# Performance work log

Hardware: AMD Instinct MI355X
Metric: run time of the kernel (lower is better)

## Reference

```python
import jax, jax.numpy as jnp
import numpy as np

B, S, D = 8, 1024, 768
H, HD = 12, 64
FF = 3072
EPS = 1e-5


def layernorm(x, w, b):
    mu = jnp.mean(x, axis=-1, keepdims=True)
    var = jnp.mean(jnp.square(x - mu), axis=-1, keepdims=True)
    return (x - mu) / jnp.sqrt(var + EPS) * w + b


def setup_inputs() -> dict:
    key = jax.random.key(0)
    ks = jax.random.split(key, 16)
    s_in = 1.0 / np.sqrt(D)
    s_p = 1.0 / np.sqrt(H * HD)
    s_ff = 1.0 / np.sqrt(FF)
    return {
        "x": jax.random.normal(ks[0], (B, S, D), dtype=jnp.float32),
        "ln1_w": jnp.ones((D,), jnp.float32),
        "ln1_b": jnp.zeros((D,), jnp.float32),
        "Wq": jax.random.uniform(ks[1], (H, D, HD), jnp.float32, -s_in, s_in),
        "bq": jax.random.uniform(ks[2], (H, HD), jnp.float32, -s_in, s_in),
        "Wk": jax.random.uniform(ks[3], (H, D, HD), jnp.float32, -s_in, s_in),
        "bk": jax.random.uniform(ks[4], (H, HD), jnp.float32, -s_in, s_in),
        "Wv": jax.random.uniform(ks[5], (H, D, HD), jnp.float32, -s_in, s_in),
        "bv": jax.random.uniform(ks[6], (H, HD), jnp.float32, -s_in, s_in),
        "Wp": jax.random.uniform(ks[7], (H * HD, D), jnp.float32, -s_p, s_p),
        "bp": jax.random.uniform(ks[8], (D,), jnp.float32, -s_p, s_p),
        "ln2_w": jnp.ones((D,), jnp.float32),
        "ln2_b": jnp.zeros((D,), jnp.float32),
        "W1": jax.random.uniform(ks[9], (D, FF), jnp.float32, -s_in, s_in),
        "b1": jax.random.uniform(ks[10], (FF,), jnp.float32, -s_in, s_in),
        "W2": jax.random.uniform(ks[11], (FF, D), jnp.float32, -s_ff, s_ff),
        "b2": jax.random.uniform(ks[12], (D,), jnp.float32, -s_ff, s_ff),
    }


def reference(x, ln1_w, ln1_b, Wq, bq, Wk, bk, Wv, bv, Wp, bp,
              ln2_w, ln2_b, W1, b1, W2, b2):
    gelu = lambda t: jax.nn.gelu(t, approximate=False)
    # --- multi-head self attention (NOTE: original never applies scale) ---
    y = layernorm(x, ln1_w, ln1_b)                       # [B,S,D]
    q = jnp.einsum('bsd,hde->bhse', y, Wq) + bq[:, None, :][None]
    k = jnp.einsum('bsd,hde->bhse', y, Wk) + bk[:, None, :][None]
    v = jnp.einsum('bsd,hde->bhse', y, Wv) + bv[:, None, :][None]
    attn = jax.nn.softmax(jnp.einsum('bhse,bhte->bhst', q, k), axis=-1)
    out = jnp.einsum('bhst,bhte->bhse', attn, v)         # [B,H,S,HD]
    out = out.transpose(0, 2, 1, 3).reshape(x.shape[0], x.shape[1], -1)  # concat heads
    y = gelu(out @ Wp + bp)                              # projection + GELU
    x = x + y                                            # residual 1
    # --- MLP block ---
    h = layernorm(x, ln2_w, ln2_b)
    h = gelu(h @ W1 + b1)
    h = gelu(h @ W2 + b2)
    return x + h                                         # residual 2
```

## Files before the change

kernel.cpp:

```cpp
#include <hip/hip_runtime.h>
#include <hip/hip_bf16.h>
#include <math.h>

#define BB 8
#define SS 1024
#define DD 768
#define HH 12
#define HDD 64
#define FFF 3072
#define NROW (BB*SS)
#define QKVN (3*DD)

typedef __hip_bfloat16 bf16;
typedef __bf16 bf16x8 __attribute__((ext_vector_type(8)));
typedef float floatx4 __attribute__((ext_vector_type(4)));

__device__ __forceinline__ float gelu_fast(float x) {
    float u = x * fmaf(0.07135481627f, x * x, 1.595769122f);
    float e = __expf(u);
    return x * e * __builtin_amdgcn_rcpf(e + 1.0f);
}

__device__ __forceinline__ unsigned short f2bfbits(float f) {
    bf16 h = __float2bfloat16(f);
    return __builtin_bit_cast(unsigned short, h);
}

__device__ __forceinline__ void gload16(const void* g, void* l) {
    __builtin_amdgcn_global_load_lds(
        (const __attribute__((address_space(1))) unsigned int*)g,
        (__attribute__((address_space(3))) unsigned int*)l, 16, 0, 0);
}

__global__ __launch_bounds__(256) void ln_kernel(const float* __restrict__ x,
                                                 const float* __restrict__ w,
                                                 const float* __restrict__ b,
                                                 bf16* __restrict__ y) {
    int row = blockIdx.x;
    const float* xr = x + (size_t)row * DD;
    bf16* yr = y + (size_t)row * DD;
    int tid = threadIdx.x;
    float v0 = xr[tid], v1 = xr[tid + 256], v2 = xr[tid + 512];
    __shared__ float red[256], red2[256];
    red[tid]  = v0 + v1 + v2;
    red2[tid] = v0*v0 + v1*v1 + v2*v2;
    __syncthreads();
    for (int off = 128; off > 0; off >>= 1) {
        if (tid < off) { red[tid] += red[tid+off]; red2[tid] += red2[tid+off]; }
        __syncthreads();
    }
    float mu  = red[0] * (1.0f / DD);
    float var = red2[0] * (1.0f / DD) - mu * mu;
    float inv = rsqrtf(var + 1e-5f);
    yr[tid]       = __float2bfloat16((v0 - mu) * inv * w[tid]       + b[tid]);
    yr[tid + 256] = __float2bfloat16((v1 - mu) * inv * w[tid + 256] + b[tid + 256]);
    yr[tid + 512] = __float2bfloat16((v2 - mu) * inv * w[tid + 512] + b[tid + 512]);
}

__global__ __launch_bounds__(256) void prep_kernel(
    const float* __restrict__ Wq, const float* __restrict__ Wk,
    const float* __restrict__ Wv, const float* __restrict__ Wp,
    const float* __restrict__ W1, const float* __restrict__ W2,
    const float* __restrict__ bq, const float* __restrict__ bk,
    const float* __restrict__ bv,
    bf16* __restrict__ Wqkvt, bf16* __restrict__ Wpt,
    bf16* __restrict__ W1t, bf16* __restrict__ W2t, float* __restrict__ bqkv)
{
    int id = blockIdx.x;
    if (id >= 6912) {
        int i = (id - 6912) * 256 + threadIdx.x;
        if (i < DD) { bqkv[i] = bq[i]; bqkv[DD + i] = bk[i]; bqkv[2*DD + i] = bv[i]; }
        return;
    }
    const float* src; bf16* dst; int K, N, hmode, local;
    if (id < 1728)      { K = DD;  N = DD;  hmode = 1; local = id % 576;
                          src = (id < 576) ? Wq : (id < 1152 ? Wk : Wv);
                          dst = Wqkvt + (size_t)(id / 576) * DD * DD; }
    else if (id < 2304) { K = DD;  N = DD;  hmode = 0; local = id - 1728; src = Wp; dst = Wpt; }
    else if (id < 4608) { K = DD;  N = FFF; hmode = 0; local = id - 2304; src = W1; dst = W1t; }
    else                { K = FFF; N = DD;  hmode = 0; local = id - 4608; src = W2; dst = W2t; }
    int ktiles = K / 32;
    int k0 = (local % ktiles) * 32, n0 = (local / ktiles) * 32;
    __shared__ float t[32][33];
    int tx = threadIdx.x & 31, ty4 = threadIdx.x >> 5;
    #pragma unroll
    for (int i = 0; i < 4; i++) {
        int k = k0 + ty4 * 4 + i;
        int n = n0 + tx;
        size_t si = hmode ? ((size_t)(n >> 6) * K * 64 + (size_t)k * 64 + (n & 63))
                          : ((size_t)k * N + n);
        t[ty4 * 4 + i][tx] = src[si];
    }
    __syncthreads();
    #pragma unroll
    for (int i = 0; i < 4; i++) {
        int n = n0 + ty4 * 4 + i;
        int k = k0 + tx;
        dst[(size_t)n * K + k] = __float2bfloat16(t[tx][ty4 * 4 + i]);
    }
}

template<int MT, int KH>
__global__ __launch_bounds__(256) void mfma_gemm(
    const bf16* __restrict__ A, const bf16* __restrict__ Bt,
    const float* __restrict__ bias, const float* __restrict__ resid,
    void* __restrict__ Cout, int M, int N, int K, int act, int out_bf16,
    int qkvmode, bf16* __restrict__ qhg, bf16* __restrict__ khg, bf16* __restrict__ vtg)
{
    constexpr int MFRAG = MT / 32;
    constexpr int ACH = MT * 4;
    __shared__ bf16 As[2][KH * MT * 32];
    __shared__ bf16 Bs[2][KH * 128 * 32];
    int tid = threadIdx.x;
    int row0 = blockIdx.y * MT, col0 = blockIdx.x * 128;
    int wave = tid >> 6, lane = tid & 63;
    int wm = (wave >> 1) * (MT / 2), wn = (wave & 1) * 64;
    int l16 = lane & 15, quad = lane >> 4;

    auto stage = [&](int k0, int buf) {
        #pragma unroll
        for (int i = 0; i < ACH * KH / 256; i++) {
            int c = tid + i * 256;
            int half = c / ACH, rem = c % ACH;
            int r = rem >> 2, pos = rem & 3;
            int ksw = k0 + half * 32 + ((pos ^ ((r >> 1) & 3)) << 3);
            gload16(A + (size_t)(row0 + r) * K + ksw, &As[buf][c * 8]);
        }
        #pragma unroll
        for (int i = 0; i < 2 * KH; i++) {
            int c = tid + i * 256;
            int half = c >> 9, rem = c & 511;
            int r = rem >> 2, pos = rem & 3;
            int ksw = k0 + half * 32 + ((pos ^ ((r >> 1) & 3)) << 3);
            gload16(Bt + (size_t)(col0 + r) * K + ksw, &Bs[buf][c * 8]);
        }
    };

    floatx4 acc[MFRAG][4] = {};

    stage(0, 0);
    int cur = 0;
    for (int k0 = 0; k0 < K; k0 += 32 * KH) {
        __syncthreads();
        if (k0 + 32 * KH < K) stage(k0 + 32 * KH, cur ^ 1);
        #pragma unroll
        for (int s = 0; s < KH; s++) {
            bf16x8 af[MFRAG], bfr[4];
            #pragma unroll
            for (int mt = 0; mt < MFRAG; mt++) {
                int r = wm + mt * 16 + l16;
                int pos = quad ^ ((r >> 1) & 3);
                af[mt] = *(const bf16x8*)&As[cur][s * MT * 32 + r * 32 + pos * 8];
            }
            #pragma unroll
            for (int nt = 0; nt < 4; nt++) {
                int r = wn + nt * 16 + l16;
                int pos = quad ^ ((r >> 1) & 3);
                bfr[nt] = *(const bf16x8*)&Bs[cur][s * 4096 + r * 32 + pos * 8];
            }
            #pragma unroll
            for (int mt = 0; mt < MFRAG; mt++)
                #pragma unroll
                for (int nt = 0; nt < 4; nt++)
                    acc[mt][nt] = __builtin_amdgcn_mfma_f32_16x16x32_bf16(
                        af[mt], bfr[nt], acc[mt][nt], 0, 0, 0);
        }
        cur ^= 1;
    }

    if (qkvmode) {
        #pragma unroll
        for (int mt = 0; mt < MFRAG; mt++) {
            int rbase = row0 + wm + mt * 16 + quad * 4;
            int bq_ = rbase >> 10, sb = rbase & 1023;
            #pragma unroll
            for (int nt = 0; nt < 4; nt++) {
                int col = col0 + wn + nt * 16 + l16;
                float bcol = bias[col];
                if (col < DD) {
                    int hh = col >> 6, e = col & 63;
                    bf16* base = qhg + (((size_t)bq_ * HH + hh) * SS + sb) * 64 + e;
                    #pragma unroll
                    for (int r = 0; r < 4; r++)
                        base[(size_t)r * 64] = __float2bfloat16(acc[mt][nt][r] + bcol);
                } else if (col < 2 * DD) {
                    int cc = col - DD, hh = cc >> 6, e = cc & 63;
                    bf16* base = khg + (((size_t)bq_ * HH + hh) * SS) * 64;
                    #pragma unroll
                    for (int r = 0; r < 4; r++) {
                        int s = sb + r;
                        int pos = (((e >> 3) ^ (s & 7)) << 3) | (e & 7);
                        base[(size_t)s * 64 + pos] = __float2bfloat16(acc[mt][nt][r] + bcol);
                    }
                } else {
                    int cc = col - 2 * DD, hh = cc >> 6, e = cc & 63;
                    int c_t = sb >> 3;
                    int sc = (c_t & ~7) | ((c_t & 7) ^ (e & 7));
                    size_t off = (((size_t)bq_ * HH + hh) * 64 + e) * SS + sc * 8 + (sb & 7);
                    ushort4 pk;
                    pk.x = f2bfbits(acc[mt][nt][0] + bcol);
                    pk.y = f2bfbits(acc[mt][nt][1] + bcol);
                    pk.z = f2bfbits(acc[mt][nt][2] + bcol);
                    pk.w = f2bfbits(acc[mt][nt][3] + bcol);
                    *(ushort4*)&vtg[off] = pk;
                }
            }
        }
        return;
    }

    #pragma unroll
    for (int mt = 0; mt < MFRAG; mt++) {
        int rbase = row0 + wm + mt * 16 + quad * 4;
        #pragma unroll
        for (int nt = 0; nt < 4; nt++) {
            int col = col0 + wn + nt * 16 + l16;
            float bcol = bias[col];
            #pragma unroll
            for (int r = 0; r < 4; r++) {
                int row = rbase + r;
                float v = acc[mt][nt][r] + bcol;
                if (act) v = gelu_fast(v);
                if (resid) v += resid[(size_t)row * N + col];
                if (out_bf16) ((bf16*)Cout)[(size_t)row * N + col] = __float2bfloat16(v);
                else          ((float*)Cout)[(size_t)row * N + col] = v;
            }
        }
    }
}

__global__ __launch_bounds__(256) void attn_mfma(
    const bf16* __restrict__ qh, const bf16* __restrict__ kh,
    const bf16* __restrict__ vT, bf16* __restrict__ ao)
{
    __shared__ bf16 Ks[2][64 * 64];
    __shared__ bf16 Vs[2][64 * 64];
    __shared__ bf16 Ps[128 * 64];

    int tid = threadIdx.x;
    int wave = tid >> 6, lane = tid & 63;
    int l16 = lane & 15, quad = lane >> 4;
    int id = blockIdx.x;
    int bh = (id & 7) * 12 + ((id >> 3) >> 3);
    int b = bh / HH, h = bh % HH;
    int s0 = ((id >> 3) & 7) * 128;
    int wm = wave * 32;

    const bf16* qbase = qh + ((size_t)bh * SS) * HDD;
    const bf16* kbase = kh + ((size_t)bh * SS) * HDD;
    const bf16* vbase = vT + ((size_t)bh * HDD) * SS;

    auto stage = [&](int t0, int buf) {
        #pragma unroll
        for (int i = 0; i < 2; i++) {
            int c = tid + i * 256;
            gload16(kbase + (size_t)t0 * 64 + c * 8, &Ks[buf][c * 8]);
            gload16(vbase + (size_t)(c >> 3) * SS + t0 + (c & 7) * 8, &Vs[buf][c * 8]);
        }
    };

    bf16x8 qf[2][2];
    #pragma unroll
    for (int mt = 0; mt < 2; mt++)
        #pragma unroll
        for (int ks = 0; ks < 2; ks++)
            qf[mt][ks] = *(const bf16x8*)(qbase +
                (size_t)(s0 + wm + mt * 16 + l16) * HDD + ks * 32 + quad * 8);

    floatx4 oaccT[4][2] = {};
    float lsum[2] = {};

    stage(0, 0);
    int cur = 0;
    for (int t0 = 0; t0 < SS; t0 += 64) {
        __syncthreads();
        if (t0 + 64 < SS) stage(t0 + 64, cur ^ 1);

        floatx4 st[4][2] = {};
        #pragma unroll
        for (int tt = 0; tt < 4; tt++) {
            int t = tt * 16 + l16;
            #pragma unroll
            for (int ks = 0; ks < 2; ks++) {
                int pos = (quad + 4 * ks) ^ (t & 7);
                bf16x8 kf = *(const bf16x8*)(&Ks[cur][t * 64 + pos * 8]);
                #pragma unroll
                for (int mt = 0; mt < 2; mt++)
                    st[tt][mt] = __builtin_amdgcn_mfma_f32_16x16x32_bf16(
                        kf, qf[mt][ks], st[tt][mt], 0, 0, 0);
            }
        }

        #pragma unroll
        for (int tt = 0; tt < 4; tt++)
            #pragma unroll
            for (int mt = 0; mt < 2; mt++) {
                float p0 = __expf(st[tt][mt][0]);
                float p1 = __expf(st[tt][mt][1]);
                float p2 = __expf(st[tt][mt][2]);
                float p3 = __expf(st[tt][mt][3]);
                lsum[mt] += (p0 + p1) + (p2 + p3);
                int m = wm + mt * 16 + l16;
                int c = tt * 2 + (quad >> 1);
                ushort4 pk;
                pk.x = f2bfbits(p0); pk.y = f2bfbits(p1);
                pk.z = f2bfbits(p2); pk.w = f2bfbits(p3);
                *(ushort4*)&Ps[m * 64 + ((c ^ (m & 7)) << 3) + (quad & 1) * 4] = pk;
            }

        #pragma unroll
        for (int ks = 0; ks < 2; ks++) {
            bf16x8 pf[2];
            #pragma unroll
            for (int mt = 0; mt < 2; mt++) {
                int m = wm + mt * 16 + l16;
                pf[mt] = *(const bf16x8*)(&Ps[m * 64 + (((quad + 4 * ks) ^ (m & 7)) << 3)]);
            }
            #pragma unroll
            for (int et = 0; et < 4; et++) {
                int e = et * 16 + l16;
                int vpos = (quad + 4 * ks) ^ (e & 7);
                bf16x8 vf = *(const bf16x8*)(&Vs[cur][e * 64 + vpos * 8]);
                #pragma unroll
                for (int mt = 0; mt < 2; mt++)
                    oaccT[et][mt] = __builtin_amdgcn_mfma_f32_16x16x32_bf16(
                        vf, pf[mt], oaccT[et][mt], 0, 0, 0);
            }
        }
        cur ^= 1;
    }

    float linv[2];
    #pragma unroll
    for (int mt = 0; mt < 2; mt++) {
        float l = lsum[mt];
        l += __shfl_xor(l, 16, 64);
        l += __shfl_xor(l, 32, 64);
        linv[mt] = __builtin_amdgcn_rcpf(l);
    }
    #pragma unroll
    for (int et = 0; et < 4; et++)
        #pragma unroll
        for (int mt = 0; mt < 2; mt++) {
            int m = wm + mt * 16 + l16;
            int c = et * 2 + (quad >> 1);
            ushort4 pk;
            pk.x = f2bfbits(oaccT[et][mt][0] * linv[mt]);
            pk.y = f2bfbits(oaccT[et][mt][1] * linv[mt]);
            pk.z = f2bfbits(oaccT[et][mt][2] * linv[mt]);
            pk.w = f2bfbits(oaccT[et][mt][3] * linv[mt]);
            *(ushort4*)&Ps[m * 64 + ((c ^ (m & 7)) << 3) + (quad & 1) * 4] = pk;
        }
    int mrow = wm + (lane >> 1);
    bf16* op = ao + ((size_t)b * SS + s0 + mrow) * DD + h * HDD;
    #pragma unroll
    for (int i = 0; i < 4; i++) {
        int j = (lane & 1) * 4 + i;
        bf16x8 v = *(const bf16x8*)&Ps[mrow * 64 + ((j ^ (mrow & 7)) << 3)];
        *(bf16x8*)&op[j * 8] = v;
    }
}

extern "C" void kernel_launch(void* const* d_in, const int* in_sizes, int n_in,
                              void* d_out, int out_size, void* d_ws, size_t ws_size,
                              hipStream_t stream)
{
    (void)in_sizes; (void)n_in; (void)out_size; (void)ws_size;
    const float* x    = (const float*)d_in[0];
    const float* ln1w = (const float*)d_in[1];
    const float* ln1b = (const float*)d_in[2];
    const float* Wq   = (const float*)d_in[3];
    const float* bq   = (const float*)d_in[4];
    const float* Wk   = (const float*)d_in[5];
    const float* bk   = (const float*)d_in[6];
    const float* Wv   = (const float*)d_in[7];
    const float* bv   = (const float*)d_in[8];
    const float* Wp   = (const float*)d_in[9];
    const float* bp   = (const float*)d_in[10];
    const float* ln2w = (const float*)d_in[11];
    const float* ln2b = (const float*)d_in[12];
    const float* W1   = (const float*)d_in[13];
    const float* b1   = (const float*)d_in[14];
    const float* W2   = (const float*)d_in[15];
    const float* b2   = (const float*)d_in[16];
    float* out = (float*)d_out;

    char* p = (char*)d_ws;
    auto alloc = [&](size_t bytes) { char* r = p; p += (bytes + 255) & ~255ull; return r; };
    bf16*  Wqkvt = (bf16*)alloc((size_t)QKVN * DD * 2);
    bf16*  Wpt   = (bf16*)alloc((size_t)DD * DD * 2);
    bf16*  W1t   = (bf16*)alloc((size_t)FFF * DD * 2);
    bf16*  W2t   = (bf16*)alloc((size_t)DD * FFF * 2);
    float* bqkv  = (float*)alloc((size_t)QKVN * 4);
    bf16*  yb    = (bf16*)alloc((size_t)NROW * DD * 2);
    char*  dynr  = alloc((size_t)NROW * DD * 2 + 3 * ((size_t)NROW * DD * 2));
    bf16*  aob   = (bf16*)dynr;
    bf16*  qhb   = (bf16*)(dynr + (size_t)NROW * DD * 2);
    bf16*  khb   = qhb + (size_t)NROW * DD;
    bf16*  vtb   = khb + (size_t)NROW * DD;
    bf16*  hb    = (bf16*)dynr;

    prep_kernel<<<6915, 256, 0, stream>>>(Wq, Wk, Wv, Wp, W1, W2, bq, bk, bv,
                                          Wqkvt, Wpt, W1t, W2t, bqkv);

    ln_kernel<<<NROW, 256, 0, stream>>>(x, ln1w, ln1b, yb);

    mfma_gemm<128,1><<<dim3(QKVN/128, NROW/128), 256, 0, stream>>>(
        yb, Wqkvt, bqkv, nullptr, nullptr, NROW, QKVN, DD, 0, 0, 1, qhb, khb, vtb);

    attn_mfma<<<dim3(BB*HH*(SS/128)), 256, 0, stream>>>(qhb, khb, vtb, aob);

    mfma_gemm<64,2><<<dim3(DD/128, NROW/64), 256, 0, stream>>>(
        aob, Wpt, bp, x, out, NROW, DD, DD, 1, 0, 0, nullptr, nullptr, nullptr);

    ln_kernel<<<NROW, 256, 0, stream>>>(out, ln2w, ln2b, yb);

    mfma_gemm<64,2><<<dim3(FFF/128, NROW/64), 256, 0, stream>>>(
        yb, W1t, b1, nullptr, hb, NROW, FFF, DD, 1, 1, 0, nullptr, nullptr, nullptr);

    mfma_gemm<64,2><<<dim3(DD/128, NROW/64), 256, 0, stream>>>(
        hb, W2t, b2, out, out, NROW, DD, FFF, 1, 0, 0, nullptr, nullptr, nullptr);
}
```

Before: 396.0 us.

## Remap GEMM blocks per XCD and store intermediate residual in bf16

GEMM launches switch to a 1D grid whose block index is decomposed so that each XCD (id & 7) owns a contiguous band of row tiles, improving L2 reuse of A and B tiles within a chiplet. The post-attention residual stream x1 is now written as bf16 into a new buffer instead of fp32 into out. LayerNorm 2 and the final GEMM's residual read from that buffer, which reduces bytes moved. This trades extra rounding error in the residual path for less memory traffic.

```diff
diff --git a/kernel.cpp b/kernel.cpp
--- a/kernel.cpp
+++ b/kernel.cpp
@@ -32,15 +32,20 @@
         (__attribute__((address_space(3))) unsigned int*)l, 16, 0, 0);
 }
 
-__global__ __launch_bounds__(256) void ln_kernel(const float* __restrict__ x,
+__device__ __forceinline__ float ld_as_float(const float* p)  { return *p; }
+__device__ __forceinline__ float ld_as_float(const bf16* p)   { return __bfloat162float(*p); }
+
+template<typename T>
+__global__ __launch_bounds__(256) void ln_kernel(const T* __restrict__ x,
                                                  const float* __restrict__ w,
                                                  const float* __restrict__ b,
                                                  bf16* __restrict__ y) {
     int row = blockIdx.x;
-    const float* xr = x + (size_t)row * DD;
+    const T* xr = x + (size_t)row * DD;
     bf16* yr = y + (size_t)row * DD;
     int tid = threadIdx.x;
-    float v0 = xr[tid], v1 = xr[tid + 256], v2 = xr[tid + 512];
+    float v0 = ld_as_float(xr + tid), v1 = ld_as_float(xr + tid + 256),
+          v2 = ld_as_float(xr + tid + 512);
     __shared__ float red[256], red2[256];
     red[tid]  = v0 + v1 + v2;
     red2[tid] = v0*v0 + v1*v1 + v2*v2;
@@ -103,8 +108,9 @@
 template<int MT, int KH>
 __global__ __launch_bounds__(256) void mfma_gemm(
     const bf16* __restrict__ A, const bf16* __restrict__ Bt,
-    const float* __restrict__ bias, const float* __restrict__ resid,
-    void* __restrict__ Cout, int M, int N, int K, int act, int out_bf16,
+    const float* __restrict__ bias, const float* __restrict__ residf,
+    const bf16* __restrict__ residb, void* __restrict__ Cout,
+    int M, int N, int K, int act, int out_bf16, int nx, int py,
     int qkvmode, bf16* __restrict__ qhg, bf16* __restrict__ khg, bf16* __restrict__ vtg)
 {
     constexpr int MFRAG = MT / 32;
@@ -112,7 +118,9 @@
     __shared__ bf16 As[2][KH * MT * 32];
     __shared__ bf16 Bs[2][KH * 128 * 32];
     int tid = threadIdx.x;
-    int row0 = blockIdx.y * MT, col0 = blockIdx.x * 128;
+    int id = blockIdx.x;
+    int xcd = id & 7, slot = id >> 3;
+    int row0 = (xcd * py + slot / nx) * MT, col0 = (slot % nx) * 128;
     int wave = tid >> 6, lane = tid & 63;
     int wm = (wave >> 1) * (MT / 2), wn = (wave & 1) * 64;
     int l16 = lane & 15, quad = lane >> 4;
@@ -221,7 +229,8 @@
                 int row = rbase + r;
                 float v = acc[mt][nt][r] + bcol;
                 if (act) v = gelu_fast(v);
-                if (resid) v += resid[(size_t)row * N + col];
+                if (residf) v += residf[(size_t)row * N + col];
+                if (residb) v += __bfloat162float(residb[(size_t)row * N + col]);
                 if (out_bf16) ((bf16*)Cout)[(size_t)row * N + col] = __float2bfloat16(v);
                 else          ((float*)Cout)[(size_t)row * N + col] = v;
             }
@@ -393,6 +402,7 @@
     bf16*  W2t   = (bf16*)alloc((size_t)DD * FFF * 2);
     float* bqkv  = (float*)alloc((size_t)QKVN * 4);
     bf16*  yb    = (bf16*)alloc((size_t)NROW * DD * 2);
+    bf16*  x1b   = (bf16*)alloc((size_t)NROW * DD * 2);
     char*  dynr  = alloc((size_t)NROW * DD * 2 + 3 * ((size_t)NROW * DD * 2));
     bf16*  aob   = (bf16*)dynr;
     bf16*  qhb   = (bf16*)(dynr + (size_t)NROW * DD * 2);
@@ -403,21 +413,25 @@
     prep_kernel<<<6915, 256, 0, stream>>>(Wq, Wk, Wv, Wp, W1, W2, bq, bk, bv,
                                           Wqkvt, Wpt, W1t, W2t, bqkv);
 
-    ln_kernel<<<NROW, 256, 0, stream>>>(x, ln1w, ln1b, yb);
-
-    mfma_gemm<128,1><<<dim3(QKVN/128, NROW/128), 256, 0, stream>>>(
-        yb, Wqkvt, bqkv, nullptr, nullptr, NROW, QKVN, DD, 0, 0, 1, qhb, khb, vtb);
+    ln_kernel<float><<<NROW, 256, 0, stream>>>(x, ln1w, ln1b, yb);
+
+    mfma_gemm<128,1><<<1152, 256, 0, stream>>>(
+        yb, Wqkvt, bqkv, nullptr, nullptr, nullptr, NROW, QKVN, DD, 0, 0, 18, 8,
+        1, qhb, khb, vtb);
 
     attn_mfma<<<dim3(BB*HH*(SS/128)), 256, 0, stream>>>(qhb, khb, vtb, aob);
 
-    mfma_gemm<64,2><<<dim3(DD/128, NROW/64), 256, 0, stream>>>(
-        aob, Wpt, bp, x, out, NROW, DD, DD, 1, 0, 0, nullptr, nullptr, nullptr);
-
-    ln_kernel<<<NROW, 256, 0, stream>>>(out, ln2w, ln2b, yb);
-
-    mfma_gemm<64,2><<<dim3(FFF/128, NROW/64), 256, 0, stream>>>(
-        yb, W1t, b1, nullptr, hb, NROW, FFF, DD, 1, 1, 0, nullptr, nullptr, nullptr);
-
-    mfma_gemm<64,2><<<dim3(DD/128, NROW/64), 256, 0, stream>>>(
-        hb, W2t, b2, out, out, NROW, DD, FFF, 1, 0, 0, nullptr, nullptr, nullptr);
-}
+    mfma_gemm<64,2><<<768, 256, 0, stream>>>(
+        aob, Wpt, bp, x, nullptr, x1b, NROW, DD, DD, 1, 1, 6, 16,
+        0, nullptr, nullptr, nullptr);
+
+    ln_kernel<bf16><<<NROW, 256, 0, stream>>>(x1b, ln2w, ln2b, yb);
+
+    mfma_gemm<64,2><<<3072, 256, 0, stream>>>(
+        yb, W1t, b1, nullptr, nullptr, hb, NROW, FFF, DD, 1, 1, 24, 16,
+        0, nullptr, nullptr, nullptr);
+
+    mfma_gemm<64,2><<<768, 256, 0, stream>>>(
+        hb, W2t, b2, nullptr, x1b, out, NROW, DD, FFF, 1, 0, 6, 16,
+        0, nullptr, nullptr, nullptr);
+}
```

Measured after the change: 378.5 us. 1.05x faster.
